# Optimization experiments

Hardware: AMD Instinct MI355X
Metric: run time of the kernel (lower is better)

Reference implementation:

```python
import jax, jax.numpy as jnp
import numpy as np

RADIUS = 0.1
MAX_NEIGHBORS = 64


def setup_inputs() -> dict:
    key0 = jax.random.key(0)
    k1, k2 = jax.random.split(key0)
    query = jax.random.uniform(k1, (4, 2048, 3), dtype=jnp.float32)
    key = jax.random.uniform(k2, (4, 8192, 3), dtype=jnp.float32)
    return {"query": query, "key": key}


def reference(query, key):
    # PointNet++-style ball query: for each query point, the indices of the
    # first MAX_NEIGHBORS key points (in key order) with squared distance
    # < RADIUS^2; remaining slots are padded with the first found neighbor
    # index (0 if no neighbor exists, matching zero-initialized CUDA output).
    B, N1, _ = query.shape
    N2 = key.shape[1]
    K = MAX_NEIGHBORS

    # [B, N1, N2] squared pairwise distances
    d2 = jnp.sum((query[:, :, None, :] - key[:, None, :, :]) ** 2, axis=-1)
    within = d2 < jnp.float32(RADIUS) ** 2  # [B, N1, N2] bool

    # slot each valid neighbor lands in (in key-index order)
    pos = jnp.cumsum(within.astype(jnp.int32), axis=-1) - 1  # [B, N1, N2]
    take = within & (pos < K)
    slot = jnp.where(take, pos, K)  # invalid entries routed to dummy slot K

    n2_idx = jnp.broadcast_to(jnp.arange(N2, dtype=jnp.int32), (B, N1, N2))
    b_idx = jnp.arange(B)[:, None, None]
    n1_idx = jnp.arange(N1)[None, :, None]

    out = jnp.full((B, N1, K + 1), -1, dtype=jnp.int32)
    # slots < K are unique per (b, n1); duplicates only at dummy slot K
    out = out.at[b_idx, n1_idx, slot].set(n2_idx)
    out = out[..., :K]  # drop dummy slot

    # pad empty slots with index of first in-radius neighbor (0 if none)
    first = jnp.argmax(within, axis=-1).astype(jnp.int32)  # [B, N1]
    out = jnp.where(out < 0, first[..., None], out)
    return out
```

## Files before the change

kernel.cpp:

```cpp
#include <hip/hip_runtime.h>


constexpr int   K    = 64;
constexpr float R2   = 0.01f;
constexpr int   B    = 4;
constexpr int   N1   = 2048;
constexpr int   N2   = 8192;
constexpr int   GC   = 5;
constexpr int   NCELL = GC * GC * GC;
constexpr float INVCELL = 5.0f;
constexpr int   SUBS       = 128;
constexpr int   SUBS_PER_B = 32;

constexpr size_t SORTED_BYTES = (size_t)B * N2 * 16;
constexpr size_t CS_BYTES     = (size_t)B * (NCELL + 1) * 4;
constexpr size_t WS_NEEDED    = SORTED_BYTES + CS_BYTES + (size_t)SUBS * NCELL * 4;

__device__ __forceinline__ int cell_of(float v) {
    int c = (int)(v * INVCELL);
    return c < 0 ? 0 : (c > GC - 1 ? GC - 1 : c);
}

__global__ __launch_bounds__(256) void hist_kernel(
    const float* __restrict__ key,
    int* __restrict__ hists)
{
    __shared__ int h[NCELL];
    const int k = blockIdx.x;
    const int t = threadIdx.x;
    if (t < NCELL) h[t] = 0;
    __syncthreads();
    const int p = k * 256 + t;
    const float x = key[p * 3 + 0];
    const float y = key[p * 3 + 1];
    const float z = key[p * 3 + 2];
    const int cell = (cell_of(x) * GC + cell_of(y)) * GC + cell_of(z);
    atomicAdd(&h[cell], 1);
    __syncthreads();
    if (t < NCELL) hists[k * NCELL + t] = h[t];
}

__global__ __launch_bounds__(256) void scatter_kernel(
    const float* __restrict__ key,
    const int* __restrict__ hists,
    int* __restrict__ cell_start,
    float4* __restrict__ sorted)
{
    __shared__ int sbuf[128];
    __shared__ int cursor[NCELL];

    const int k = blockIdx.x;
    const int b = k >> 5;
    const int s = k & 31;
    const int t = threadIdx.x;

    int mybase = 0, total = 0;
    if (t < NCELL) {
        const int* hb = hists + (b * SUBS_PER_B) * NCELL + t;
        int acc = 0;
        #pragma unroll
        for (int s2 = 0; s2 < SUBS_PER_B; ++s2) {
            if (s2 == s) mybase = acc;
            acc += hb[s2 * NCELL];
        }
        total = acc;
    }

    if (t < 128) sbuf[t] = (t < NCELL) ? total : 0;
    __syncthreads();
    for (int off = 1; off < 128; off <<= 1) {
        int v = 0;
        if (t < 128 && t >= off) v = sbuf[t - off];
        __syncthreads();
        if (t < 128) sbuf[t] += v;
        __syncthreads();
    }
    if (t < NCELL) {
        const int excl = sbuf[t] - total;
        cursor[t] = excl + mybase;
        if (s == 0) {
            cell_start[b * (NCELL + 1) + t + 1] = sbuf[t];
            if (t == 0) cell_start[b * (NCELL + 1)] = 0;
        }
    }
    __syncthreads();

    const int p = k * 256 + t;
    const float x = key[p * 3 + 0];
    const float y = key[p * 3 + 1];
    const float z = key[p * 3 + 2];
    const int cell = (cell_of(x) * GC + cell_of(y)) * GC + cell_of(z);
    const int pos  = atomicAdd(&cursor[cell], 1);
    float4 v;
    v.x = x; v.y = y; v.z = z; v.w = __int_as_float(p & (N2 - 1));
    sorted[(size_t)b * N2 + pos] = v;
}

__global__ __launch_bounds__(256) void ballquery_grid_kernel(
    const float* __restrict__ query,
    const float4* __restrict__ sorted,
    const int* __restrict__ cell_start,
    int* __restrict__ out)
{
    __shared__ unsigned int bm[4 * 256];

    const int lane = threadIdx.x & 63;
    const int wv   = threadIdx.x >> 6;
    const int q    = blockIdx.x * 4 + wv;
    const int b    = q >> 11;

    const float qx = query[q * 3 + 0];
    const float qy = query[q * 3 + 1];
    const float qz = query[q * 3 + 2];

    const float ux = qx * INVCELL, uy = qy * INVCELL, uz = qz * INVCELL;
    const int cx = cell_of(qx), cy = cell_of(qy), cz = cell_of(qz);
    const int nx = (ux - cx < 0.5f) ? cx - 1 : cx + 1;
    const int ny = (uy - cy < 0.5f) ? cy - 1 : cy + 1;
    const int nz = (uz - cz < 0.5f) ? cz - 1 : cz + 1;
    const int xlo = max(0, min(cx, nx)), xhi = min(GC - 1, max(cx, nx));
    const int ylo = max(0, min(cy, ny)), yhi = min(GC - 1, max(cy, ny));
    const int zlo = max(0, min(cz, nz)), zhi = min(GC - 1, max(cz, nz));

    unsigned int* wbm = bm + wv * 256;
    uint4 zz; zz.x = zz.y = zz.z = zz.w = 0u;
    ((uint4*)wbm)[lane] = zz;
    __threadfence_block();

    const int*    cs = cell_start + b * (NCELL + 1);
    const float4* sb = sorted + (size_t)b * N2;

    for (int xx = xlo; xx <= xhi; ++xx) {
        for (int yy = ylo; yy <= yhi; ++yy) {
            const int colz = (xx * GC + yy) * GC;
            const int s = cs[colz + zlo];
            const int e = cs[colz + zhi + 1];
            for (int t0 = s; t0 < e; t0 += 64) {
                const int i = t0 + lane;
                const float4 kv = sb[min(i, e - 1)];
                const float dx = kv.x - qx;
                const float dy = kv.y - qy;
                const float dz = kv.z - qz;
                const bool within = (i < e) && (dx * dx + dy * dy + dz * dz < R2);
                if (within) {
                    const int id = __float_as_int(kv.w);
                    atomicOr(&wbm[id >> 5], 1u << (id & 31));
                }
            }
        }
    }
    __threadfence_block();

    const uint4 w = ((const uint4*)wbm)[lane];
    const int c = __popc(w.x) + __popc(w.y) + __popc(w.z) + __popc(w.w);

    int x = c;
    #pragma unroll
    for (int off = 1; off < 64; off <<= 1) {
        int y = __shfl_up(x, off);
        if (lane >= off) x += y;
    }
    const int base = x - c;
    const int cnt  = __shfl(x, 63);

    int fs;
    if      (w.x) fs = __builtin_ctz(w.x);
    else if (w.y) fs = 32 + __builtin_ctz(w.y);
    else if (w.z) fs = 64 + __builtin_ctz(w.z);
    else if (w.w) fs = 96 + __builtin_ctz(w.w);
    else          fs = 0;
    int myfirst = c ? (lane << 7) + fs : 0x7fffffff;
    #pragma unroll
    for (int off = 32; off; off >>= 1)
        myfirst = min(myfirst, __shfl_xor(myfirst, off));
    const int firstIdx = (cnt == 0) ? 0 : myfirst;

    int* op = out + q * K;
    int slot = base;
    unsigned int wr[4] = {w.x, w.y, w.z, w.w};
    #pragma unroll
    for (int r = 0; r < 4; ++r) {
        unsigned int m = wr[r];
        const int bb = (lane << 7) + (r << 5);
        while (m) {
            const int bp = __builtin_ctz(m);
            m &= m - 1;
            if (slot < K) op[slot] = bb + bp;
            ++slot;
        }
    }

    const int kpad = cnt < K ? cnt : K;
    const int s2 = kpad + lane;
    if (s2 < K) op[s2] = firstIdx;
}

__global__ __launch_bounds__(256) void ballquery_bruteforce_kernel(
    const float* __restrict__ query, const float* __restrict__ key,
    int* __restrict__ out)
{
    const int lane = threadIdx.x & 63;
    const int q = blockIdx.x * 4 + (threadIdx.x >> 6);
    const int b = q >> 11;
    const float qx = query[q * 3], qy = query[q * 3 + 1], qz = query[q * 3 + 2];
    const float* kb = key + (size_t)b * N2 * 3;
    int* op = out + (size_t)q * K;
    int count = 0, first = 0;
    bool have_first = false;
    const unsigned long long lane_mask_lt = (lane == 0) ? 0ull : (~0ull >> (64 - lane));
    for (int c = 0; c < N2 / 64; ++c) {
        if (count >= K) break;
        const int j = (c << 6) + lane;
        const float* kp = kb + j * 3;
        const float dx = kp[0] - qx, dy = kp[1] - qy, dz = kp[2] - qz;
        const bool within = dx * dx + dy * dy + dz * dz < R2;
        const unsigned long long mask = __ballot(within);
        if (mask) {
            if (!have_first) { first = (c << 6) + __builtin_ctzll(mask); have_first = true; }
            if (within) {
                const int slot = count + __popcll(mask & lane_mask_lt);
                if (slot < K) op[slot] = j;
            }
            count += __popcll(mask);
        }
    }
    const int cnt = count < K ? count : K;
    if (cnt + lane < K) op[cnt + lane] = first;
}

extern "C" void kernel_launch(void* const* d_in, const int* in_sizes, int n_in,
                              void* d_out, int out_size, void* d_ws, size_t ws_size,
                              hipStream_t stream) {
    const float* query = (const float*)d_in[0];
    const float* key   = (const float*)d_in[1];
    int* out = (int*)d_out;

    if (ws_size < WS_NEEDED) {
        ballquery_bruteforce_kernel<<<(B * N1) / 4, 256, 0, stream>>>(query, key, out);
        return;
    }

    float4* sorted     = (float4*)d_ws;
    int*    cell_start = (int*)((char*)d_ws + SORTED_BYTES);
    int*    hists      = (int*)((char*)d_ws + SORTED_BYTES + CS_BYTES);

    hist_kernel<<<SUBS, 256, 0, stream>>>(key, hists);
    scatter_kernel<<<SUBS, 256, 0, stream>>>(key, hists, cell_start, sorted);
    ballquery_grid_kernel<<<(B * N1) / 4, 256, 0, stream>>>(query, sorted, cell_start, out);
}
```

Measured before the change: 68.20 us.

## Fuse histogram and scatter into one build kernel that recomputes batch histograms

Replaces the separate histogram and scatter kernels with a single build kernel. Each block rereads all keys of its batch to compute the full-batch and prefix cell histograms in shared memory, which removes one launch and the global histogram buffer. The cost is 32x redundant key reads and shared atomics per batch. It also drops the block-level thread fences around the per-wave bitmap, which relies on wave-level ordering of LDS accesses for correctness.

```diff
diff --git a/kernel.cpp b/kernel.cpp
--- a/kernel.cpp
+++ b/kernel.cpp
@@ -9,43 +9,25 @@
 constexpr int   GC   = 5;
 constexpr int   NCELL = GC * GC * GC;
 constexpr float INVCELL = 5.0f;
-constexpr int   SUBS       = 128;
 constexpr int   SUBS_PER_B = 32;
+constexpr int   SUBS       = B * SUBS_PER_B;
 
 constexpr size_t SORTED_BYTES = (size_t)B * N2 * 16;
 constexpr size_t CS_BYTES     = (size_t)B * (NCELL + 1) * 4;
-constexpr size_t WS_NEEDED    = SORTED_BYTES + CS_BYTES + (size_t)SUBS * NCELL * 4;
+constexpr size_t WS_NEEDED    = SORTED_BYTES + CS_BYTES;
 
 __device__ __forceinline__ int cell_of(float v) {
     int c = (int)(v * INVCELL);
     return c < 0 ? 0 : (c > GC - 1 ? GC - 1 : c);
 }
 
-__global__ __launch_bounds__(256) void hist_kernel(
+__global__ __launch_bounds__(256) void build_kernel(
     const float* __restrict__ key,
-    int* __restrict__ hists)
-{
-    __shared__ int h[NCELL];
-    const int k = blockIdx.x;
-    const int t = threadIdx.x;
-    if (t < NCELL) h[t] = 0;
-    __syncthreads();
-    const int p = k * 256 + t;
-    const float x = key[p * 3 + 0];
-    const float y = key[p * 3 + 1];
-    const float z = key[p * 3 + 2];
-    const int cell = (cell_of(x) * GC + cell_of(y)) * GC + cell_of(z);
-    atomicAdd(&h[cell], 1);
-    __syncthreads();
-    if (t < NCELL) hists[k * NCELL + t] = h[t];
-}
-
-__global__ __launch_bounds__(256) void scatter_kernel(
-    const float* __restrict__ key,
-    const int* __restrict__ hists,
     int* __restrict__ cell_start,
     float4* __restrict__ sorted)
 {
+    __shared__ int h_tot[NCELL];
+    __shared__ int h_pre[NCELL];
     __shared__ int sbuf[128];
     __shared__ int cursor[NCELL];
 
@@ -54,19 +36,26 @@
     const int s = k & 31;
     const int t = threadIdx.x;
 
-    int mybase = 0, total = 0;
-    if (t < NCELL) {
-        const int* hb = hists + (b * SUBS_PER_B) * NCELL + t;
-        int acc = 0;
-        #pragma unroll
-        for (int s2 = 0; s2 < SUBS_PER_B; ++s2) {
-            if (s2 == s) mybase = acc;
-            acc += hb[s2 * NCELL];
-        }
-        total = acc;
-    }
-
-    if (t < 128) sbuf[t] = (t < NCELL) ? total : 0;
+    if (t < NCELL) { h_tot[t] = 0; h_pre[t] = 0; }
+    __syncthreads();
+
+    const float* kb = key + (size_t)b * N2 * 3;
+    float mx = 0.f, my = 0.f, mz = 0.f;
+    int mycell = 0;
+    for (int i = 0; i < SUBS_PER_B; ++i) {
+        const int j = i * 256 + t;
+        const float x = kb[j * 3 + 0];
+        const float y = kb[j * 3 + 1];
+        const float z = kb[j * 3 + 2];
+        const int c = (cell_of(x) * GC + cell_of(y)) * GC + cell_of(z);
+        atomicAdd(&h_tot[c], 1);
+        if (i < s) atomicAdd(&h_pre[c], 1);
+        if (i == s) { mx = x; my = y; mz = z; mycell = c; }
+    }
+    __syncthreads();
+
+    const int total = (t < NCELL) ? h_tot[t] : 0;
+    if (t < 128) sbuf[t] = total;
     __syncthreads();
     for (int off = 1; off < 128; off <<= 1) {
         int v = 0;
@@ -77,7 +66,7 @@
     }
     if (t < NCELL) {
         const int excl = sbuf[t] - total;
-        cursor[t] = excl + mybase;
+        cursor[t] = excl + h_pre[t];
         if (s == 0) {
             cell_start[b * (NCELL + 1) + t + 1] = sbuf[t];
             if (t == 0) cell_start[b * (NCELL + 1)] = 0;
@@ -85,14 +74,9 @@
     }
     __syncthreads();
 
-    const int p = k * 256 + t;
-    const float x = key[p * 3 + 0];
-    const float y = key[p * 3 + 1];
-    const float z = key[p * 3 + 2];
-    const int cell = (cell_of(x) * GC + cell_of(y)) * GC + cell_of(z);
-    const int pos  = atomicAdd(&cursor[cell], 1);
+    const int pos = atomicAdd(&cursor[mycell], 1);
     float4 v;
-    v.x = x; v.y = y; v.z = z; v.w = __int_as_float(p & (N2 - 1));
+    v.x = mx; v.y = my; v.z = mz; v.w = __int_as_float(s * 256 + t);
     sorted[(size_t)b * N2 + pos] = v;
 }
 
@@ -125,7 +109,6 @@
     unsigned int* wbm = bm + wv * 256;
     uint4 zz; zz.x = zz.y = zz.z = zz.w = 0u;
     ((uint4*)wbm)[lane] = zz;
-    __threadfence_block();
 
     const int*    cs = cell_start + b * (NCELL + 1);
     const float4* sb = sorted + (size_t)b * N2;
@@ -149,7 +132,6 @@
             }
         }
     }
-    __threadfence_block();
 
     const uint4 w = ((const uint4*)wbm)[lane];
     const int c = __popc(w.x) + __popc(w.y) + __popc(w.z) + __popc(w.w);
@@ -242,9 +224,7 @@
 
     float4* sorted     = (float4*)d_ws;
     int*    cell_start = (int*)((char*)d_ws + SORTED_BYTES);
-    int*    hists      = (int*)((char*)d_ws + SORTED_BYTES + CS_BYTES);
-
-    hist_kernel<<<SUBS, 256, 0, stream>>>(key, hists);
-    scatter_kernel<<<SUBS, 256, 0, stream>>>(key, hists, cell_start, sorted);
+
+    build_kernel<<<SUBS, 256, 0, stream>>>(key, cell_start, sorted);
     ballquery_grid_kernel<<<(B * N1) / 4, 256, 0, stream>>>(query, sorted, cell_start, out);
 }
```

Measured after the change: 76.09 us. +11.6%, slower.

## Fuse histogram and scatter kernels using inter-block flag synchronisation

Applied to the files above, without the earlier changes.

Merges the histogram and scatter kernels into one launch. Each block publishes its per-block histogram, then spin-waits on release/acquire flags from the other blocks of the same batch before doing the prefix scan and scatter. Each key point's coordinates and cell are computed once and kept in registers instead of being reloaded. It also drops the block-level fences around the LDS bitmap in the query kernel. This removes a kernel launch and its gap, but relies on all 128 blocks being resident at once. Flags keep a constant value across calls and are never reset, so later calls can pass the wait before the current histograms are written.

```diff
diff --git a/kernel.cpp b/kernel.cpp
--- a/kernel.cpp
+++ b/kernel.cpp
@@ -12,22 +12,42 @@
 constexpr int   SUBS       = 128;
 constexpr int   SUBS_PER_B = 32;
 
+constexpr unsigned FLAG_BASE = 0xA1B2C300u;
+
 constexpr size_t SORTED_BYTES = (size_t)B * N2 * 16;
 constexpr size_t CS_BYTES     = (size_t)B * (NCELL + 1) * 4;
-constexpr size_t WS_NEEDED    = SORTED_BYTES + CS_BYTES + (size_t)SUBS * NCELL * 4;
+constexpr size_t HIST_BYTES   = (size_t)SUBS * NCELL * 4;
+constexpr size_t WS_NEEDED    = SORTED_BYTES + CS_BYTES + HIST_BYTES + SUBS * 4;
 
 __device__ __forceinline__ int cell_of(float v) {
     int c = (int)(v * INVCELL);
     return c < 0 ? 0 : (c > GC - 1 ? GC - 1 : c);
 }
 
-__global__ __launch_bounds__(256) void hist_kernel(
+__device__ __forceinline__ unsigned agent_load_acq(const unsigned* p) {
+    return __hip_atomic_load(p, __ATOMIC_ACQUIRE, __HIP_MEMORY_SCOPE_AGENT);
+}
+__device__ __forceinline__ void agent_store_rel(unsigned* p, unsigned v) {
+    __hip_atomic_store(p, v, __ATOMIC_RELEASE, __HIP_MEMORY_SCOPE_AGENT);
+}
+
+
+__global__ __launch_bounds__(256) void build_fused_kernel(
     const float* __restrict__ key,
-    int* __restrict__ hists)
+    int* __restrict__ hists,
+    unsigned* __restrict__ flags,
+    int* __restrict__ cell_start,
+    float4* __restrict__ sorted)
 {
     __shared__ int h[NCELL];
+    __shared__ int sbuf[128];
+    __shared__ int cursor[NCELL];
+
     const int k = blockIdx.x;
+    const int b = k >> 5;
+    const int s = k & 31;
     const int t = threadIdx.x;
+
     if (t < NCELL) h[t] = 0;
     __syncthreads();
     const int p = k * 256 + t;
@@ -38,21 +58,16 @@
     atomicAdd(&h[cell], 1);
     __syncthreads();
     if (t < NCELL) hists[k * NCELL + t] = h[t];
-}
-
-__global__ __launch_bounds__(256) void scatter_kernel(
-    const float* __restrict__ key,
-    const int* __restrict__ hists,
-    int* __restrict__ cell_start,
-    float4* __restrict__ sorted)
-{
-    __shared__ int sbuf[128];
-    __shared__ int cursor[NCELL];
-
-    const int k = blockIdx.x;
-    const int b = k >> 5;
-    const int s = k & 31;
-    const int t = threadIdx.x;
+
+    __threadfence();
+    __syncthreads();
+    if (t == 0) agent_store_rel(&flags[k], FLAG_BASE | (unsigned)k);
+    if (t < SUBS_PER_B) {
+        const int src = b * SUBS_PER_B + t;
+        const unsigned want = FLAG_BASE | (unsigned)src;
+        while (agent_load_acq(&flags[src]) != want) {  }
+    }
+    __syncthreads();
 
     int mybase = 0, total = 0;
     if (t < NCELL) {
@@ -85,16 +100,12 @@
     }
     __syncthreads();
 
-    const int p = k * 256 + t;
-    const float x = key[p * 3 + 0];
-    const float y = key[p * 3 + 1];
-    const float z = key[p * 3 + 2];
-    const int cell = (cell_of(x) * GC + cell_of(y)) * GC + cell_of(z);
-    const int pos  = atomicAdd(&cursor[cell], 1);
+    const int pos = atomicAdd(&cursor[cell], 1);
     float4 v;
     v.x = x; v.y = y; v.z = z; v.w = __int_as_float(p & (N2 - 1));
     sorted[(size_t)b * N2 + pos] = v;
 }
+
 
 __global__ __launch_bounds__(256) void ballquery_grid_kernel(
     const float* __restrict__ query,
@@ -125,7 +136,6 @@
     unsigned int* wbm = bm + wv * 256;
     uint4 zz; zz.x = zz.y = zz.z = zz.w = 0u;
     ((uint4*)wbm)[lane] = zz;
-    __threadfence_block();
 
     const int*    cs = cell_start + b * (NCELL + 1);
     const float4* sb = sorted + (size_t)b * N2;
@@ -149,7 +159,6 @@
             }
         }
     }
-    __threadfence_block();
 
     const uint4 w = ((const uint4*)wbm)[lane];
     const int c = __popc(w.x) + __popc(w.y) + __popc(w.z) + __popc(w.w);
@@ -240,11 +249,11 @@
         return;
     }
 
-    float4* sorted     = (float4*)d_ws;
-    int*    cell_start = (int*)((char*)d_ws + SORTED_BYTES);
-    int*    hists      = (int*)((char*)d_ws + SORTED_BYTES + CS_BYTES);
-
-    hist_kernel<<<SUBS, 256, 0, stream>>>(key, hists);
-    scatter_kernel<<<SUBS, 256, 0, stream>>>(key, hists, cell_start, sorted);
+    float4*   sorted     = (float4*)d_ws;
+    int*      cell_start = (int*)((char*)d_ws + SORTED_BYTES);
+    int*      hists      = (int*)((char*)d_ws + SORTED_BYTES + CS_BYTES);
+    unsigned* flags      = (unsigned*)((char*)d_ws + SORTED_BYTES + CS_BYTES + HIST_BYTES);
+
+    build_fused_kernel<<<SUBS, 256, 0, stream>>>(key, hists, flags, cell_start, sorted);
     ballquery_grid_kernel<<<(B * N1) / 4, 256, 0, stream>>>(query, sorted, cell_start, out);
 }
```

Measured after the change: 78.79 us. 1.16x slower.
